# Kernel optimization log

Hardware: AMD Instinct MI355X
Metric: run time of the kernel (lower is better)

## Reference

```python
import jax, jax.numpy as jnp
import numpy as np

EPS = 1e-05


def setup_inputs() -> dict:
    key = jax.random.key(0)
    kx, = jax.random.split(key, 1)
    B, C, T = 8, 512, 8192
    x = jax.random.normal(kx, (B, C, T), dtype=jnp.float32)
    weight = jnp.ones((1, C, 1), dtype=jnp.float32)
    bias = jnp.zeros((1, C, 1), dtype=jnp.float32)
    return {"x": x, "weight": weight, "bias": bias}


def reference(x, weight, bias):
    # x: [B, C, T]; causal (running) per-channel mean/var over time.
    T = x.shape[-1]
    count = jnp.arange(1, T + 1, dtype=x.dtype)  # [T], broadcasts over B,C
    cumsum = jnp.cumsum(x, axis=-1)
    cumsum_sq = jnp.cumsum(x * x, axis=-1)
    mean = cumsum / count
    var = cumsum_sq / count - mean * mean
    x_norm = (x - mean) * jax.lax.rsqrt(var + EPS)
    return x_norm * weight + bias
```

## Files before the change

### kernel.cpp

```cpp
#include <hip/hip_runtime.h>
#include <math.h>

#define EPS 1e-5f

__device__ __forceinline__ int swz(int a) { return a ^ ((a >> 3) & 7); }

__global__ __launch_bounds__(512, 8) void causal_ln_kernel(
    const float* __restrict__ x,
    const float* __restrict__ weight,
    const float* __restrict__ bias,
    float* __restrict__ out,
    int C, int T)
{
    __shared__ float lds[2048 * 4];
    __shared__ float wsum[8], wsum2[8];

    const int row  = blockIdx.x;
    const int c    = row % C;
    const float wv = weight[c];
    const float bv = bias[c];
    const long long base = (long long)row * (long long)T;

    const int t    = threadIdx.x;
    const int lane = t & 63;
    const int wid  = t >> 6;

    const float* xrow = x + base;
#pragma unroll
    for (int j = 0; j < 4; ++j) {
        int slot = j * 512 + t;
        int g    = swz(slot);
        const __attribute__((address_space(1))) float* gp =
            (const __attribute__((address_space(1))) float*)(xrow + g * 4);
        __attribute__((address_space(3))) float* lp =
            (__attribute__((address_space(3))) float*)(&lds[(j * 512 + (wid << 6)) * 4]);
        __builtin_amdgcn_global_load_lds(gp, lp, 16, 0, 0);
    }
    __syncthreads();

    float4 v[4];
#pragma unroll
    for (int j = 0; j < 4; ++j)
        v[j] = *(const float4*)&lds[swz(t * 4 + j) * 4];

    float s = 0.f, s2 = 0.f;
#pragma unroll
    for (int j = 0; j < 4; ++j) {
        s  += v[j].x + v[j].y + v[j].z + v[j].w;
        s2 += v[j].x * v[j].x + v[j].y * v[j].y
            + v[j].z * v[j].z + v[j].w * v[j].w;
    }

    float ws = s, ws2 = s2;
#pragma unroll
    for (int off = 1; off < 64; off <<= 1) {
        float a  = __shfl_up(ws,  off, 64);
        float a2 = __shfl_up(ws2, off, 64);
        if (lane >= off) { ws += a; ws2 += a2; }
    }

    if (lane == 63) { wsum[wid] = ws; wsum2[wid] = ws2; }
    __syncthreads();
    float off1 = 0.f, off2 = 0.f;
#pragma unroll
    for (int k = 0; k < 8; ++k) {
        if (k < wid) { off1 += wsum[k]; off2 += wsum2[k]; }
    }

    float es  = __shfl_up(ws,  1, 64);
    float es2 = __shfl_up(ws2, 1, 64);
    if (lane == 0) { es = 0.f; es2 = 0.f; }
    float run  = off1 + es;
    float run2 = off2 + es2;

    float cnt = (float)(t * 16);
#pragma unroll
    for (int j = 0; j < 4; ++j) {
        float xs[4] = {v[j].x, v[j].y, v[j].z, v[j].w};
#pragma unroll
        for (int i = 0; i < 4; ++i) {
            float xi = xs[i];
            run  += xi;
            run2 += xi * xi;
            cnt  += 1.f;
            float rc   = __builtin_amdgcn_rcpf(cnt);
            float mean = run * rc;
            float var  = fmaxf(run2 * rc - mean * mean, 0.f);
            float rinv = __builtin_amdgcn_rsqf(var + EPS);
            xs[i] = (xi - mean) * rinv * wv + bv;
        }
        *(float4*)&lds[swz(t * 4 + j) * 4] =
            make_float4(xs[0], xs[1], xs[2], xs[3]);
    }
    __syncthreads();

    float4* og = (float4*)(out + base);
#pragma unroll
    for (int j = 0; j < 4; ++j) {
        int g = j * 512 + t;
        og[g] = *(const float4*)&lds[swz(g) * 4];
    }
}

extern "C" void kernel_launch(void* const* d_in, const int* in_sizes, int n_in,
                              void* d_out, int out_size, void* d_ws, size_t ws_size,
                              hipStream_t stream) {
    const float* x      = (const float*)d_in[0];
    const float* weight = (const float*)d_in[1];
    const float* bias   = (const float*)d_in[2];
    float* out          = (float*)d_out;

    const int C = in_sizes[1];
    const int T = 8192;
    const int rows = in_sizes[0] / T;

    dim3 grid(rows), block(512);
    hipLaunchKernelGGL(causal_ln_kernel, grid, block, 0, stream,
                       x, weight, bias, out, C, T);
}
```

Before: 234.4 us.

## Process eight rows per block with double-buffered async LDS prefetch

Each block now handles eight consecutive rows and prefetches the next row into a second LDS buffer with global_load_lds while the current row is scanned, so load latency can overlap compute. Reciprocals of the running counts are computed once per thread and reused across rows. Results are written straight from registers instead of being staged back through LDS. The trade-offs are fewer blocks and lower occupancy (launch bounds drop to 2), and per-thread 64-byte strided stores that are less coalesced than the old LDS-staged writes.

```diff
diff --git a/kernel.cpp b/kernel.cpp
--- a/kernel.cpp
+++ b/kernel.cpp
@@ -2,103 +2,119 @@
 #include <math.h>
 
 #define EPS 1e-5f
+#define T_LEN 8192
+#define ROWS_PER_BLOCK 8
 
 __device__ __forceinline__ int swz(int a) { return a ^ ((a >> 3) & 7); }
 
-__global__ __launch_bounds__(512, 8) void causal_ln_kernel(
+__global__ __launch_bounds__(512, 2) void causal_ln_kernel(
     const float* __restrict__ x,
     const float* __restrict__ weight,
     const float* __restrict__ bias,
     float* __restrict__ out,
     int C, int T)
 {
-    __shared__ float lds[2048 * 4];
+    __shared__ float lds[2][T_LEN];
     __shared__ float wsum[8], wsum2[8];
-
-    const int row  = blockIdx.x;
-    const int c    = row % C;
-    const float wv = weight[c];
-    const float bv = bias[c];
-    const long long base = (long long)row * (long long)T;
 
     const int t    = threadIdx.x;
     const int lane = t & 63;
     const int wid  = t >> 6;
+    const int row0 = blockIdx.x * ROWS_PER_BLOCK;
 
-    const float* xrow = x + base;
+    float rc[16];
 #pragma unroll
-    for (int j = 0; j < 4; ++j) {
-        int slot = j * 512 + t;
-        int g    = swz(slot);
-        const __attribute__((address_space(1))) float* gp =
-            (const __attribute__((address_space(1))) float*)(xrow + g * 4);
-        __attribute__((address_space(3))) float* lp =
-            (__attribute__((address_space(3))) float*)(&lds[(j * 512 + (wid << 6)) * 4]);
-        __builtin_amdgcn_global_load_lds(gp, lp, 16, 0, 0);
-    }
-    __syncthreads();
+    for (int k = 0; k < 16; ++k)
+        rc[k] = __builtin_amdgcn_rcpf((float)(t * 16 + k + 1));
 
-    float4 v[4];
+    auto stage = [&](int b, int r) {
+        const float* xrow = x + (long long)(row0 + r) * (long long)T_LEN;
 #pragma unroll
-    for (int j = 0; j < 4; ++j)
-        v[j] = *(const float4*)&lds[swz(t * 4 + j) * 4];
+        for (int j = 0; j < 4; ++j) {
+            int slot = j * 512 + t;
+            int g    = swz(slot);
+            const __attribute__((address_space(1))) float* gp =
+                (const __attribute__((address_space(1))) float*)(xrow + g * 4);
+            __attribute__((address_space(3))) float* lp =
+                (__attribute__((address_space(3))) float*)
+                    (&lds[b][(j * 512 + (wid << 6)) * 4]);
+            __builtin_amdgcn_global_load_lds(gp, lp, 16, 0, 0);
+        }
+    };
 
-    float s = 0.f, s2 = 0.f;
+    stage(0, 0);
+
+    for (int r = 0; r < ROWS_PER_BLOCK; ++r) {
+        const int cur = r & 1;
+        if (r + 1 < ROWS_PER_BLOCK)
+            stage(cur ^ 1, r + 1);
+
+        asm volatile("s_waitcnt vmcnt(4)" ::: "memory");
+        __builtin_amdgcn_s_barrier();
+
+        float4 v[4];
 #pragma unroll
-    for (int j = 0; j < 4; ++j) {
-        s  += v[j].x + v[j].y + v[j].z + v[j].w;
-        s2 += v[j].x * v[j].x + v[j].y * v[j].y
-            + v[j].z * v[j].z + v[j].w * v[j].w;
-    }
+        for (int j = 0; j < 4; ++j)
+            v[j] = *(const float4*)&lds[cur][swz(t * 4 + j) * 4];
 
-    float ws = s, ws2 = s2;
+        float s = 0.f, s2 = 0.f;
 #pragma unroll
-    for (int off = 1; off < 64; off <<= 1) {
-        float a  = __shfl_up(ws,  off, 64);
-        float a2 = __shfl_up(ws2, off, 64);
-        if (lane >= off) { ws += a; ws2 += a2; }
-    }
+        for (int j = 0; j < 4; ++j) {
+            s  += v[j].x + v[j].y + v[j].z + v[j].w;
+            s2 += v[j].x * v[j].x + v[j].y * v[j].y
+                + v[j].z * v[j].z + v[j].w * v[j].w;
+        }
 
-    if (lane == 63) { wsum[wid] = ws; wsum2[wid] = ws2; }
-    __syncthreads();
-    float off1 = 0.f, off2 = 0.f;
+        float ws = s, ws2 = s2;
 #pragma unroll
-    for (int k = 0; k < 8; ++k) {
-        if (k < wid) { off1 += wsum[k]; off2 += wsum2[k]; }
-    }
+        for (int off = 1; off < 64; off <<= 1) {
+            float a  = __shfl_up(ws,  off, 64);
+            float a2 = __shfl_up(ws2, off, 64);
+            if (lane >= off) { ws += a; ws2 += a2; }
+        }
 
-    float es  = __shfl_up(ws,  1, 64);
-    float es2 = __shfl_up(ws2, 1, 64);
-    if (lane == 0) { es = 0.f; es2 = 0.f; }
-    float run  = off1 + es;
-    float run2 = off2 + es2;
+        if (lane == 63) { wsum[wid] = ws; wsum2[wid] = ws2; }
+        asm volatile("s_waitcnt lgkmcnt(0)" ::: "memory");
+        __builtin_amdgcn_s_barrier();
 
-    float cnt = (float)(t * 16);
+        float off1 = 0.f, off2 = 0.f;
 #pragma unroll
-    for (int j = 0; j < 4; ++j) {
-        float xs[4] = {v[j].x, v[j].y, v[j].z, v[j].w};
+        for (int k = 0; k < 8; ++k) {
+            if (k < wid) { off1 += wsum[k]; off2 += wsum2[k]; }
+        }
+
+        float es  = __shfl_up(ws,  1, 64);
+        float es2 = __shfl_up(ws2, 1, 64);
+        if (lane == 0) { es = 0.f; es2 = 0.f; }
+        float run  = off1 + es;
+        float run2 = off2 + es2;
+
+        const int   row = row0 + r;
+        const float wv  = weight[row % C];
+        const float bv  = bias[row % C];
+
+        float4 o[4];
 #pragma unroll
-        for (int i = 0; i < 4; ++i) {
-            float xi = xs[i];
-            run  += xi;
-            run2 += xi * xi;
-            cnt  += 1.f;
-            float rc   = __builtin_amdgcn_rcpf(cnt);
-            float mean = run * rc;
-            float var  = fmaxf(run2 * rc - mean * mean, 0.f);
-            float rinv = __builtin_amdgcn_rsqf(var + EPS);
-            xs[i] = (xi - mean) * rinv * wv + bv;
+        for (int j = 0; j < 4; ++j) {
+            float xs[4] = {v[j].x, v[j].y, v[j].z, v[j].w};
+#pragma unroll
+            for (int i = 0; i < 4; ++i) {
+                float xi = xs[i];
+                run  += xi;
+                run2 += xi * xi;
+                float rcv  = rc[j * 4 + i];
+                float mean = run * rcv;
+                float var  = fmaxf(run2 * rcv - mean * mean, 0.f);
+                float rinv = __builtin_amdgcn_rsqf(var + EPS);
+                xs[i] = (xi - mean) * rinv * wv + bv;
+            }
+            o[j] = make_float4(xs[0], xs[1], xs[2], xs[3]);
         }
-        *(float4*)&lds[swz(t * 4 + j) * 4] =
-            make_float4(xs[0], xs[1], xs[2], xs[3]);
-    }
-    __syncthreads();
 
-    float4* og = (float4*)(out + base);
+        float4* og = (float4*)(out + (long long)row * (long long)T_LEN + t * 16);
 #pragma unroll
-    for (int j = 0; j < 4; ++j) {
-        int g = j * 512 + t;
-        og[g] = *(const float4*)&lds[swz(g) * 4];
+        for (int j = 0; j < 4; ++j)
+            og[j] = o[j];
     }
 }
 
@@ -114,7 +130,7 @@
     const int T = 8192;
     const int rows = in_sizes[0] / T;
 
-    dim3 grid(rows), block(512);
+    dim3 grid(rows / ROWS_PER_BLOCK), block(512);
     hipLaunchKernelGGL(causal_ln_kernel, grid, block, 0, stream,
                        x, weight, bias, out, C, T);
 }
```

Measured after the change: 244.0 us. 4.1% more time.

## Drop LDS staging; scan four strided segments directly from coalesced global loads

Applied to the files above, without the earlier changes.

Removes the LDS transpose through global_load_lds and the LDS round-trip for output. Each thread now loads coalesced float4s at stride 512 and does four independent block-wide prefix scans, one per segment, combining them with segment totals. Loads and stores go straight to and from registers, saving LDS traffic and a barrier. In exchange it does four times the shuffle scan work, uses more registers, and lowers the launch bounds occupancy hint from 8 to 4.

```diff
diff --git a/kernel.cpp b/kernel.cpp
--- a/kernel.cpp
+++ b/kernel.cpp
@@ -2,80 +2,90 @@
 #include <math.h>
 
 #define EPS 1e-5f
+#define T_LEN 8192
 
-__device__ __forceinline__ int swz(int a) { return a ^ ((a >> 3) & 7); }
-
-__global__ __launch_bounds__(512, 8) void causal_ln_kernel(
+__global__ __launch_bounds__(512, 4) void causal_ln_kernel(
     const float* __restrict__ x,
     const float* __restrict__ weight,
     const float* __restrict__ bias,
     float* __restrict__ out,
-    int C, int T)
+    int C)
 {
-    __shared__ float lds[2048 * 4];
-    __shared__ float wsum[8], wsum2[8];
-
-    const int row  = blockIdx.x;
-    const int c    = row % C;
-    const float wv = weight[c];
-    const float bv = bias[c];
-    const long long base = (long long)row * (long long)T;
+    __shared__ float4 wsumS[8], wsumQ[8];
 
     const int t    = threadIdx.x;
     const int lane = t & 63;
     const int wid  = t >> 6;
+    const int row  = blockIdx.x;
 
-    const float* xrow = x + base;
+    const float4* xg = (const float4*)(x + (long long)row * T_LEN);
+    float4 v[4];
+#pragma unroll
+    for (int j = 0; j < 4; ++j)
+        v[j] = xg[j * 512 + t];
+
+    float gs[4], gq[4];
 #pragma unroll
     for (int j = 0; j < 4; ++j) {
-        int slot = j * 512 + t;
-        int g    = swz(slot);
-        const __attribute__((address_space(1))) float* gp =
-            (const __attribute__((address_space(1))) float*)(xrow + g * 4);
-        __attribute__((address_space(3))) float* lp =
-            (__attribute__((address_space(3))) float*)(&lds[(j * 512 + (wid << 6)) * 4]);
-        __builtin_amdgcn_global_load_lds(gp, lp, 16, 0, 0);
+        gs[j] = v[j].x + v[j].y + v[j].z + v[j].w;
+        gq[j] = v[j].x * v[j].x + v[j].y * v[j].y
+              + v[j].z * v[j].z + v[j].w * v[j].w;
+    }
+
+    float ws[4], wq[4];
+#pragma unroll
+    for (int j = 0; j < 4; ++j) { ws[j] = gs[j]; wq[j] = gq[j]; }
+#pragma unroll
+    for (int off = 1; off < 64; off <<= 1) {
+#pragma unroll
+        for (int j = 0; j < 4; ++j) {
+            float a = __shfl_up(ws[j], off, 64);
+            float b = __shfl_up(wq[j], off, 64);
+            if (lane >= off) { ws[j] += a; wq[j] += b; }
+        }
+    }
+
+    if (lane == 63) {
+        wsumS[wid] = make_float4(ws[0], ws[1], ws[2], ws[3]);
+        wsumQ[wid] = make_float4(wq[0], wq[1], wq[2], wq[3]);
     }
     __syncthreads();
 
-    float4 v[4];
+    float woS[4] = {0.f,0.f,0.f,0.f}, woQ[4] = {0.f,0.f,0.f,0.f};
+    float rtS[4] = {0.f,0.f,0.f,0.f}, rtQ[4] = {0.f,0.f,0.f,0.f};
 #pragma unroll
-    for (int j = 0; j < 4; ++j)
-        v[j] = *(const float4*)&lds[swz(t * 4 + j) * 4];
+    for (int w = 0; w < 8; ++w) {
+        float4 a = wsumS[w], b = wsumQ[w];
+        float am[4] = {a.x, a.y, a.z, a.w};
+        float bm[4] = {b.x, b.y, b.z, b.w};
+#pragma unroll
+        for (int j = 0; j < 4; ++j) {
+            rtS[j] += am[j]; rtQ[j] += bm[j];
+            if (w < wid) { woS[j] += am[j]; woQ[j] += bm[j]; }
+        }
+    }
 
-    float s = 0.f, s2 = 0.f;
+    float es[4], eq[4];
 #pragma unroll
     for (int j = 0; j < 4; ++j) {
-        s  += v[j].x + v[j].y + v[j].z + v[j].w;
-        s2 += v[j].x * v[j].x + v[j].y * v[j].y
-            + v[j].z * v[j].z + v[j].w * v[j].w;
+        es[j] = __shfl_up(ws[j], 1, 64);
+        eq[j] = __shfl_up(wq[j], 1, 64);
+    }
+    if (lane == 0) {
+#pragma unroll
+        for (int j = 0; j < 4; ++j) { es[j] = 0.f; eq[j] = 0.f; }
     }
 
-    float ws = s, ws2 = s2;
-#pragma unroll
-    for (int off = 1; off < 64; off <<= 1) {
-        float a  = __shfl_up(ws,  off, 64);
-        float a2 = __shfl_up(ws2, off, 64);
-        if (lane >= off) { ws += a; ws2 += a2; }
-    }
+    const float wv = weight[row % C];
+    const float bv = bias[row % C];
+    float4* og = (float4*)(out + (long long)row * T_LEN);
 
-    if (lane == 63) { wsum[wid] = ws; wsum2[wid] = ws2; }
-    __syncthreads();
-    float off1 = 0.f, off2 = 0.f;
-#pragma unroll
-    for (int k = 0; k < 8; ++k) {
-        if (k < wid) { off1 += wsum[k]; off2 += wsum2[k]; }
-    }
-
-    float es  = __shfl_up(ws,  1, 64);
-    float es2 = __shfl_up(ws2, 1, 64);
-    if (lane == 0) { es = 0.f; es2 = 0.f; }
-    float run  = off1 + es;
-    float run2 = off2 + es2;
-
-    float cnt = (float)(t * 16);
+    float rp = 0.f, rq = 0.f;
 #pragma unroll
     for (int j = 0; j < 4; ++j) {
+        float run  = rp + woS[j] + es[j];
+        float run2 = rq + woQ[j] + eq[j];
+        float cnt  = (float)(4 * (j * 512 + t));
         float xs[4] = {v[j].x, v[j].y, v[j].z, v[j].w};
 #pragma unroll
         for (int i = 0; i < 4; ++i) {
@@ -83,22 +93,14 @@
             run  += xi;
             run2 += xi * xi;
             cnt  += 1.f;
-            float rc   = __builtin_amdgcn_rcpf(cnt);
-            float mean = run * rc;
-            float var  = fmaxf(run2 * rc - mean * mean, 0.f);
+            float rcv  = __builtin_amdgcn_rcpf(cnt);
+            float mean = run * rcv;
+            float var  = fmaxf(run2 * rcv - mean * mean, 0.f);
             float rinv = __builtin_amdgcn_rsqf(var + EPS);
             xs[i] = (xi - mean) * rinv * wv + bv;
         }
-        *(float4*)&lds[swz(t * 4 + j) * 4] =
-            make_float4(xs[0], xs[1], xs[2], xs[3]);
-    }
-    __syncthreads();
-
-    float4* og = (float4*)(out + base);
-#pragma unroll
-    for (int j = 0; j < 4; ++j) {
-        int g = j * 512 + t;
-        og[g] = *(const float4*)&lds[swz(g) * 4];
+        og[j * 512 + t] = make_float4(xs[0], xs[1], xs[2], xs[3]);
+        rp += rtS[j]; rq += rtQ[j];
     }
 }
 
@@ -116,5 +118,5 @@
 
     dim3 grid(rows), block(512);
     hipLaunchKernelGGL(causal_ln_kernel, grid, block, 0, stream,
-                       x, weight, bias, out, C, T);
+                       x, weight, bias, out, C);
 }
```

New measurement: 234.4 us. Within noise of the previous version (-0.0%).

## Process each row with one wavefront using chunked scans and register prefetch

Applied to the files above, without the earlier changes.

Each row of 8192 elements is now handled by a single 64-lane wave that walks 32 chunks of float4 in turn. Each chunk gets a wave-level shuffle scan, and the running offset is carried forward with readlane. This removes the LDS staging, the block-wide barriers and the cross-wave offset exchange. A 4-deep register prefetch of upcoming chunks is meant to hide global load latency. The cost is a serial dependency across 32 chunks within each wave and 32 shuffle scans per row instead of one.

```diff
diff --git a/kernel.cpp b/kernel.cpp
--- a/kernel.cpp
+++ b/kernel.cpp
@@ -2,103 +2,77 @@
 #include <math.h>
 
 #define EPS 1e-5f
+#define T_LEN 8192
+#define WAVES_PER_BLOCK 4
 
-__device__ __forceinline__ int swz(int a) { return a ^ ((a >> 3) & 7); }
-
-__global__ __launch_bounds__(512, 8) void causal_ln_kernel(
+__global__ __launch_bounds__(256, 8) void causal_ln_kernel(
     const float* __restrict__ x,
     const float* __restrict__ weight,
     const float* __restrict__ bias,
     float* __restrict__ out,
-    int C, int T)
+    int C)
 {
-    __shared__ float lds[2048 * 4];
-    __shared__ float wsum[8], wsum2[8];
-
-    const int row  = blockIdx.x;
-    const int c    = row % C;
-    const float wv = weight[c];
-    const float bv = bias[c];
-    const long long base = (long long)row * (long long)T;
-
     const int t    = threadIdx.x;
     const int lane = t & 63;
     const int wid  = t >> 6;
+    const int row  = blockIdx.x * WAVES_PER_BLOCK + wid;
 
-    const float* xrow = x + base;
-#pragma unroll
-    for (int j = 0; j < 4; ++j) {
-        int slot = j * 512 + t;
-        int g    = swz(slot);
-        const __attribute__((address_space(1))) float* gp =
-            (const __attribute__((address_space(1))) float*)(xrow + g * 4);
-        __attribute__((address_space(3))) float* lp =
-            (__attribute__((address_space(3))) float*)(&lds[(j * 512 + (wid << 6)) * 4]);
-        __builtin_amdgcn_global_load_lds(gp, lp, 16, 0, 0);
-    }
-    __syncthreads();
+    const float wv = weight[row % C];
+    const float bv = bias[row % C];
 
-    float4 v[4];
+    const float4* xg = (const float4*)(x   + (long long)row * T_LEN);
+    float4*       og = (float4*)(out + (long long)row * T_LEN);
+
+    float4 buf[4];
 #pragma unroll
     for (int j = 0; j < 4; ++j)
-        v[j] = *(const float4*)&lds[swz(t * 4 + j) * 4];
+        buf[j] = xg[j * 64 + lane];
 
-    float s = 0.f, s2 = 0.f;
+    float off1 = 0.f, off2 = 0.f;
+
 #pragma unroll
-    for (int j = 0; j < 4; ++j) {
-        s  += v[j].x + v[j].y + v[j].z + v[j].w;
-        s2 += v[j].x * v[j].x + v[j].y * v[j].y
-            + v[j].z * v[j].z + v[j].w * v[j].w;
-    }
+    for (int c = 0; c < 32; ++c) {
+        float4 cur = buf[c & 3];
+        if (c + 4 < 32)
+            buf[c & 3] = xg[(c + 4) * 64 + lane];
 
-    float ws = s, ws2 = s2;
+        float s  = cur.x + cur.y + cur.z + cur.w;
+        float s2 = cur.x * cur.x + cur.y * cur.y
+                 + cur.z * cur.z + cur.w * cur.w;
+
+        float ws = s, ws2 = s2;
 #pragma unroll
-    for (int off = 1; off < 64; off <<= 1) {
-        float a  = __shfl_up(ws,  off, 64);
-        float a2 = __shfl_up(ws2, off, 64);
-        if (lane >= off) { ws += a; ws2 += a2; }
-    }
+        for (int o = 1; o < 64; o <<= 1) {
+            float a = __shfl_up(ws,  o, 64);
+            float b = __shfl_up(ws2, o, 64);
+            if (lane >= o) { ws += a; ws2 += b; }
+        }
 
-    if (lane == 63) { wsum[wid] = ws; wsum2[wid] = ws2; }
-    __syncthreads();
-    float off1 = 0.f, off2 = 0.f;
-#pragma unroll
-    for (int k = 0; k < 8; ++k) {
-        if (k < wid) { off1 += wsum[k]; off2 += wsum2[k]; }
-    }
+        float es  = __shfl_up(ws,  1, 64);
+        float es2 = __shfl_up(ws2, 1, 64);
+        if (lane == 0) { es = 0.f; es2 = 0.f; }
 
-    float es  = __shfl_up(ws,  1, 64);
-    float es2 = __shfl_up(ws2, 1, 64);
-    if (lane == 0) { es = 0.f; es2 = 0.f; }
-    float run  = off1 + es;
-    float run2 = off2 + es2;
+        float run  = off1 + es;
+        float run2 = off2 + es2;
+        float cnt  = (float)((c * 64 + lane) * 4);
 
-    float cnt = (float)(t * 16);
-#pragma unroll
-    for (int j = 0; j < 4; ++j) {
-        float xs[4] = {v[j].x, v[j].y, v[j].z, v[j].w};
+        float xs[4] = {cur.x, cur.y, cur.z, cur.w};
 #pragma unroll
         for (int i = 0; i < 4; ++i) {
             float xi = xs[i];
             run  += xi;
             run2 += xi * xi;
             cnt  += 1.f;
-            float rc   = __builtin_amdgcn_rcpf(cnt);
-            float mean = run * rc;
-            float var  = fmaxf(run2 * rc - mean * mean, 0.f);
+            float rcv  = __builtin_amdgcn_rcpf(cnt);
+            float mean = run * rcv;
+            float var  = fmaxf(run2 * rcv - mean * mean, 0.f);
             float rinv = __builtin_amdgcn_rsqf(var + EPS);
             xs[i] = (xi - mean) * rinv * wv + bv;
         }
-        *(float4*)&lds[swz(t * 4 + j) * 4] =
-            make_float4(xs[0], xs[1], xs[2], xs[3]);
-    }
-    __syncthreads();
+        og[c * 64 + lane] = make_float4(xs[0], xs[1], xs[2], xs[3]);
 
-    float4* og = (float4*)(out + base);
-#pragma unroll
-    for (int j = 0; j < 4; ++j) {
-        int g = j * 512 + t;
-        og[g] = *(const float4*)&lds[swz(g) * 4];
+        off1 += __int_as_float(__builtin_amdgcn_readlane(__float_as_int(ws),  63));
+        off2 += __int_as_float(__builtin_amdgcn_readlane(__float_as_int(ws2), 63));
     }
 }
 
@@ -114,7 +88,7 @@
     const int T = 8192;
     const int rows = in_sizes[0] / T;
 
-    dim3 grid(rows), block(512);
+    dim3 grid(rows / WAVES_PER_BLOCK), block(64 * WAVES_PER_BLOCK);
     hipLaunchKernelGGL(causal_ln_kernel, grid, block, 0, stream,
-                       x, weight, bias, out, C, T);
+                       x, weight, bias, out, C);
 }
```

Result: no change. 238.9 us (+1.9%).
